# Performance work log

Measured on AMD Instinct MI355X. Metric: run time of the kernel, lower is better.

The kernel has to match this reference:

```python
import jax, jax.numpy as jnp
import numpy as np

N = 50000   # nodes
E = 800000  # edges (avg degree 16)
F = 16      # input node feature dim
H = 64      # hidden_channels
G = 128     # number of graphs
L = 3       # num_layers
OUT = 8     # output_channels


def _glorot(key, shape):
    fan = shape[-2] + shape[-1]
    return jax.random.normal(key, shape, dtype=jnp.float32) * jnp.sqrt(2.0 / fan)


def setup_inputs() -> dict:
    key = jax.random.key(0)
    ks = jax.random.split(key, 16)
    z = lambda *s: jnp.zeros(s, jnp.float32)
    return {
        "x": jax.random.normal(ks[0], (N, F), jnp.float32),
        "pos": jax.random.normal(ks[1], (N, 3), jnp.float32),
        "edge_index": jax.random.randint(ks[2], (2, E), 0, N),
        "batch": jnp.sort(jax.random.randint(ks[3], (N,), 0, G)),
        "node_W1": _glorot(ks[4], (F, H)), "node_b1": z(H),
        "node_W2": _glorot(ks[5], (H, H)), "node_b2": z(H),
        "local_W1": _glorot(ks[6], (L, 2 * H + 3, H)), "local_b1": z(L, H),
        "local_W2": _glorot(ks[7], (L, H, H)), "local_b2": z(L, H),
        "global_W1": _glorot(ks[8], (L, H, H)), "global_b1": z(L, H),
        "global_W2": _glorot(ks[9], (L, H, H)), "global_b2": z(L, H),
        "lin1_W": _glorot(ks[10], (H, H // 2)), "lin1_b": z(H // 2),
        "lin2_W": _glorot(ks[11], (H // 2, OUT)), "lin2_b": z(OUT),
    }


def reference(x, pos, edge_index, batch,
              node_W1, node_b1, node_W2, node_b2,
              local_W1, local_b1, local_W2, local_b2,
              global_W1, global_b1, global_W2, global_b2,
              lin1_W, lin1_b, lin2_W, lin2_b):
    n = x.shape[0]
    src, dst = edge_index[0], edge_index[1]  # x_j = x[src], x_i = x[dst]
    # node_lin: Linear -> ReLU -> Linear
    h = jnp.maximum(x @ node_W1 + node_b1, 0.0) @ node_W2 + node_b2
    for l in range(L):
        # message: cat([x_i, x_j, pos_j]) -> local_nn (Linear, ReLU, Linear)
        m = jnp.concatenate([h[dst], h[src], pos[src]], axis=-1)  # [E, 2H+3]
        m = jnp.maximum(m @ local_W1[l] + local_b1[l], 0.0) @ local_W2[l] + local_b2[l]
        # aggregate: scatter-add over destination nodes
        agg = jax.ops.segment_sum(m, dst, num_segments=n)
        # global_nn (Linear, ReLU, Linear), then outer ReLU from forward loop
        h = jnp.maximum(agg @ global_W1[l] + global_b1[l], 0.0) @ global_W2[l] + global_b2[l]
        h = jnp.maximum(h, 0.0)
    h = jnp.maximum(h @ lin1_W + lin1_b, 0.0)
    out = h @ lin2_W + lin2_b  # [N, OUT]
    # graph readout: scatter-add over batch ids
    return jax.ops.segment_sum(out, batch, num_segments=G)  # [G, OUT]
```

## Files before the change

kernel.cpp:

```cpp
#include <hip/hip_runtime.h>

#define N_NODES 50000
#define N_EDGES 800000
#define NGRAPH  128
#define XPITCH  72
#define NB      391
#define HEPB    4096
#define SEPB    8192
#define NGRP    3125

typedef short bf16x8 __attribute__((ext_vector_type(8)));
typedef float f32x4  __attribute__((ext_vector_type(4)));


__device__ __forceinline__ float atomAddF(float* p, float v) {
#if defined(__gfx950__) || defined(__AMDGCN__)
    return unsafeAtomicAdd(p, v);
#else
    return atomicAdd(p, v);
#endif
}

__device__ __forceinline__ unsigned short f2bf(float x) {
    unsigned u = __builtin_bit_cast(unsigned, x);
    u += 0x7fffu + ((u >> 16) & 1u);
    return (unsigned short)(u >> 16);
}
__device__ __forceinline__ float bf2f(unsigned short h) {
    return __builtin_bit_cast(float, (unsigned)h << 16);
}

__device__ __forceinline__ f32x4 mk4(float b) { f32x4 a = {b, b, b, b}; return a; }

template<int NKC, int KROW>
__device__ __forceinline__ f32x4 w_tile(const bf16x8* a,
                                        const unsigned short* __restrict__ Wm,
                                        int nt, int col, int quad, f32x4 acc) {
    const unsigned short* wp = Wm + (nt * 16 + col) * KROW + quad * 8;
#pragma unroll
    for (int c = 0; c < NKC; ++c) {
        bf16x8 b = *(const bf16x8*)(wp + c * 32);
        acc = __builtin_amdgcn_mfma_f32_16x16x32_bf16(a[c], b, acc, 0, 0, 0);
    }
    return acc;
}

template<int NKC>
__device__ __forceinline__ void a_load(const unsigned short* __restrict__ sl,
                                       int col, int quad, bf16x8* a) {
    a[0] = *(const bf16x8*)(sl + col * XPITCH + quad * 8);
    if (NKC > 1) a[1] = *(const bf16x8*)(sl + col * XPITCH + quad * 8 + 32);
}

__device__ __forceinline__ void w_store1(unsigned short* __restrict__ sl,
                                         int wv, int col, int quad, f32x4 acc,
                                         bool relu) {
#pragma unroll
    for (int r = 0; r < 4; ++r) {
        float x = acc[r];
        if (relu) x = fmaxf(x, 0.f);
        sl[(quad * 4 + r) * XPITCH + wv * 16 + col] = f2bf(x);
    }
}

__device__ __forceinline__ void g_store1(unsigned short* __restrict__ g, int gn0,
                                         int wv, int col, int quad, f32x4 acc) {
#pragma unroll
    for (int r = 0; r < 4; ++r) {
        int node = gn0 + quad * 4 + r;
        if (node < N_NODES)
            g[(size_t)node * 64 + wv * 16 + col] = f2bf(acc[r]);
    }
}

#define OFF_NW1T  0
#define OFF_NW2T  2048
#define OFF_LYR   6144
#define LYR_SZ    20480
#define OFF_LIN1T 67584
#define OFF_LIN2T 69632
#define WT_TOTAL  70144

__global__ __launch_bounds__(256) void kPrep(
    const float* __restrict__ nW1, const float* __restrict__ nW2,
    const float* __restrict__ lW1, const float* __restrict__ lW2,
    const float* __restrict__ gW1, const float* __restrict__ gW2,
    const float* __restrict__ lin1W, const float* __restrict__ lin2W,
    unsigned short* __restrict__ WT, int* __restrict__ gHist,
    float* __restrict__ out) {
    int i = blockIdx.x * 256 + threadIdx.x;
    if (blockIdx.x == 0) {
        for (int k = threadIdx.x; k < NB; k += 256) gHist[k] = 0;
        for (int k = threadIdx.x; k < NGRAPH * 8; k += 256) out[k] = 0.f;
    }
    if (i >= WT_TOTAL) return;
    int j = i;
    if (j < 2048) {
        int n = j >> 5, k = j & 31;
        WT[i] = (k < 16) ? f2bf(nW1[k * 64 + n]) : 0;
        return;
    }
    j -= 2048;
    if (j < 4096) {
        int n = j >> 6, k = j & 63;
        WT[i] = f2bf(nW2[k * 64 + n]);
        return;
    }
    j -= 4096;
    if (j < 3 * LYR_SZ) {
        int l = j / LYR_SZ;  j -= l * LYR_SZ;
        int m = j >> 12;     j &= 4095;
        int n = j >> 6, k = j & 63;
        const float* src;
        if (m == 0)      src = lW1 + (size_t)l * 131 * 64;
        else if (m == 1) src = lW1 + (size_t)l * 131 * 64 + 64 * 64;
        else if (m == 2) src = lW2 + (size_t)l * 4096;
        else if (m == 3) src = gW1 + (size_t)l * 4096;
        else             src = gW2 + (size_t)l * 4096;
        WT[i] = f2bf(src[k * 64 + n]);
        return;
    }
    j -= 3 * LYR_SZ;
    if (j < 2048) {
        int n = j >> 6, k = j & 63;
        WT[i] = f2bf(lin1W[k * 32 + n]);
        return;
    }
    j -= 2048;
    {
        int n = j >> 5, k = j & 31;
        WT[i] = (n < 8) ? f2bf(lin2W[k * 8 + n]) : 0;
    }
}

__global__ __launch_bounds__(256) void kHist(const int* __restrict__ ei,
                                             int* __restrict__ gHist) {
    __shared__ int h[NB];
    int tid = threadIdx.x;
    for (int i = tid; i < NB; i += 256) h[i] = 0;
    __syncthreads();
    int base = blockIdx.x * HEPB;
#pragma unroll
    for (int k = 0; k < HEPB; k += 256) {
        int e = base + k + tid;
        if (e < N_EDGES) atomicAdd(&h[ei[N_EDGES + e] >> 7], 1);
    }
    __syncthreads();
    for (int i = tid; i < NB; i += 256)
        if (h[i]) atomicAdd(&gHist[i], h[i]);
}

__global__ __launch_bounds__(256) void kScanB(const int* __restrict__ gHist,
                                              int* __restrict__ bucketOff,
                                              int* __restrict__ cursor) {
    __shared__ int s0[512], s1[512];
    int tid = threadIdx.x;
    for (int e = tid; e < 512; e += 256) s0[e] = (e < NB) ? gHist[e] : 0;
    __syncthreads();
    int* sp = s0; int* dp = s1;
    for (int off = 1; off < 512; off <<= 1) {
        for (int e = tid; e < 512; e += 256)
            dp[e] = sp[e] + ((e >= off) ? sp[e - off] : 0);
        __syncthreads();
        int* t = sp; sp = dp; dp = t;
    }
    for (int e = tid; e < NB; e += 256) {
        int excl = sp[e] - gHist[e];
        bucketOff[e] = excl;
        cursor[e] = excl;
    }
    if (tid == 0) bucketOff[NB] = sp[NB - 1];
}

__global__ __launch_bounds__(256) void kScat(const int* __restrict__ ei,
                                             int* __restrict__ cursor,
                                             int* __restrict__ packs) {
    __shared__ int sdata[SEPB];
    __shared__ int hist[NB];
    __shared__ int loff[NB + 1];
    __shared__ int gbase[NB];
    __shared__ int sc0[512], sc1[512];
    int tid = threadIdx.x;
    int base = blockIdx.x * SEPB;
    int nE = min(SEPB, N_EDGES - base);

    for (int i = tid; i < NB; i += 256) hist[i] = 0;
    __syncthreads();

    int myPack[SEPB / 256];
    unsigned short myRank[SEPB / 256];
#pragma unroll
    for (int kk = 0; kk < SEPB / 256; ++kk) {
        int e = base + kk * 256 + tid;
        if (e < N_EDGES) {
            int s = ei[e], d = ei[N_EDGES + e];
            myPack[kk] = (s << 16) | d;
            myRank[kk] = (unsigned short)atomicAdd(&hist[d >> 7], 1);
        }
    }
    __syncthreads();

    for (int e = tid; e < 512; e += 256) sc0[e] = (e < NB) ? hist[e] : 0;
    __syncthreads();
    int* sp = sc0; int* dp = sc1;
    for (int off = 1; off < 512; off <<= 1) {
        for (int e = tid; e < 512; e += 256)
            dp[e] = sp[e] + ((e >= off) ? sp[e - off] : 0);
        __syncthreads();
        int* t = sp; sp = dp; dp = t;
    }
    for (int e = tid; e < NB; e += 256) loff[e] = sp[e] - hist[e];
    if (tid == 0) loff[NB] = sp[NB - 1];
    __syncthreads();

    for (int e = tid; e < NB; e += 256)
        gbase[e] = hist[e] ? atomicAdd(&cursor[e], hist[e]) : 0;
#pragma unroll
    for (int kk = 0; kk < SEPB / 256; ++kk) {
        int e = base + kk * 256 + tid;
        if (e < N_EDGES) {
            int p = myPack[kk];
            int b = (p & 0xffff) >> 7;
            sdata[loff[b] + myRank[kk]] = p;
        }
    }
    __syncthreads();

    for (int i = tid; i < nE; i += 256) {
        int p = sdata[i];
        int b = (p & 0xffff) >> 7;
        packs[gbase[b] + (i - loff[b])] = p;
    }
}

__global__ __launch_bounds__(256) void kSortA(
    const int* __restrict__ bucketOff, const int* __restrict__ packs,
    unsigned short* __restrict__ srcList, int* __restrict__ rowPtr,
    const float* __restrict__ x, const float* __restrict__ pos,
    const unsigned short* __restrict__ WT,
    const float* __restrict__ nb1, const float* __restrict__ nb2,
    const float* __restrict__ lW1f, const float* __restrict__ lb1,
    unsigned short* __restrict__ u, unsigned short* __restrict__ v) {
    __shared__ int hist[128];
    __shared__ int cur[128];
    __shared__ int sc0[128], sc1[128];
    __shared__ unsigned short SL[16 * XPITCH];
    __shared__ float pw[48];

    int tid = threadIdx.x;
    if (blockIdx.x < NB) {
        int nbk = blockIdx.x;
        int nodeBase = nbk * 128;
        int nvalid = min(128, N_NODES - nodeBase);
        int eb = bucketOff[nbk], ee = bucketOff[nbk + 1];

        if (tid < 128) hist[tid] = 0;
        __syncthreads();
        for (int i = eb + tid; i < ee; i += 256)
            atomicAdd(&hist[packs[i] & 127], 1);
        __syncthreads();

        if (tid < 128) sc0[tid] = hist[tid];
        __syncthreads();
        int* sp = sc0; int* dp = sc1;
        for (int off = 1; off < 128; off <<= 1) {
            if (tid < 128) dp[tid] = sp[tid] + ((tid >= off) ? sp[tid - off] : 0);
            __syncthreads();
            int* t = sp; sp = dp; dp = t;
        }
        if (tid < 128) {
            int excl = eb + sp[tid] - hist[tid];
            if (tid < nvalid) rowPtr[nodeBase + tid] = excl;
            cur[tid] = excl;
        }
        if (nbk == NB - 1 && tid == 0) rowPtr[N_NODES] = ee;
        __syncthreads();

        for (int i = eb + tid; i < ee; i += 256) {
            int p = packs[i];
            int ps = atomicAdd(&cur[p & 127], 1);
            srcList[ps] = (unsigned short)(((unsigned)p) >> 16);
        }
        return;
    }

    int gn0 = (blockIdx.x - NB) * 16;
    int lane = tid & 63;
    int wv = __builtin_amdgcn_readfirstlane(tid >> 6);
    int col = lane & 15, quad = lane >> 4;

    for (int idx = tid; idx < 512; idx += 256) {
        int m = idx >> 5, k = idx & 31;
        int node = gn0 + m;
        float val = (k < 16 && node < N_NODES) ? x[(size_t)node * 16 + k] : 0.f;
        SL[m * XPITCH + k] = f2bf(val);
    }
    if (tid < 48) {
        int node = gn0 + tid / 3;
        pw[tid] = (node < N_NODES) ? pos[(size_t)node * 3 + tid % 3] : 0.f;
    }
    __syncthreads();

    bf16x8 a[2];
    f32x4 acc;

    a_load<1>(SL, col, quad, a);
    acc = w_tile<1, 32>(a, WT + OFF_NW1T, wv, col, quad, mk4(nb1[wv * 16 + col]));
    __syncthreads();
    w_store1(SL, wv, col, quad, acc, true);
    __syncthreads();

    a_load<2>(SL, col, quad, a);
    acc = w_tile<2, 64>(a, WT + OFF_NW2T, wv, col, quad, mk4(nb2[wv * 16 + col]));
    __syncthreads();
    w_store1(SL, wv, col, quad, acc, false);
    __syncthreads();

    const unsigned short* aT = WT + OFF_LYR;
    const unsigned short* bT = aT + 4096;
    const float* W1c = lW1f + 128 * 64;

    a_load<2>(SL, col, quad, a);
    acc = w_tile<2, 64>(a, aT, wv, col, quad, mk4(0.f));
    g_store1(u, gn0, wv, col, quad, acc);

    int ch = wv * 16 + col;
    acc = w_tile<2, 64>(a, bT, wv, col, quad, mk4(lb1[ch]));
    float w0 = W1c[ch], w1 = W1c[64 + ch], w2 = W1c[128 + ch];
#pragma unroll
    for (int r = 0; r < 4; ++r) {
        int rr = quad * 4 + r;
        acc[r] += pw[rr * 3 + 0] * w0 + pw[rr * 3 + 1] * w1 + pw[rr * 3 + 2] * w2;
    }
    g_store1(v, gn0, wv, col, quad, acc);
}

__global__ __launch_bounds__(256) void kAgg(const int* __restrict__ rowPtr,
                                            const unsigned short* __restrict__ srcList,
                                            const unsigned short* __restrict__ u,
                                            const unsigned short* __restrict__ v,
                                            unsigned short* __restrict__ aggH) {
    int gt = blockIdx.x * 256 + threadIdx.x;
    int n = gt >> 6;
    int lane = gt & 63;
    if (n >= N_NODES) return;
    int sub = lane & 15;
    int q = lane >> 4;

    ushort4 uu = *(const ushort4*)(u + (size_t)n * 64 + sub * 4);
    float u0 = bf2f(uu.x), u1 = bf2f(uu.y), u2 = bf2f(uu.z), u3 = bf2f(uu.w);

    int b = rowPtr[n], e = rowPtr[n + 1];
    int deg = e - b;
    int full16 = deg & ~15;
    float a0 = 0.f, a1 = 0.f, a2 = 0.f, a3 = 0.f;

    for (int g0 = 0; g0 < full16; g0 += 16) {
        int i = b + g0 + 4 * q;
        int s0 = srcList[i];
        int s1 = srcList[i + 1];
        int s2 = srcList[i + 2];
        int s3 = srcList[i + 3];
        ushort4 w0 = *(const ushort4*)(v + (size_t)s0 * 64 + sub * 4);
        ushort4 w1 = *(const ushort4*)(v + (size_t)s1 * 64 + sub * 4);
        ushort4 w2 = *(const ushort4*)(v + (size_t)s2 * 64 + sub * 4);
        ushort4 w3 = *(const ushort4*)(v + (size_t)s3 * 64 + sub * 4);
        a0 += fmaxf(u0 + bf2f(w0.x), 0.f) + fmaxf(u0 + bf2f(w1.x), 0.f)
            + fmaxf(u0 + bf2f(w2.x), 0.f) + fmaxf(u0 + bf2f(w3.x), 0.f);
        a1 += fmaxf(u1 + bf2f(w0.y), 0.f) + fmaxf(u1 + bf2f(w1.y), 0.f)
            + fmaxf(u1 + bf2f(w2.y), 0.f) + fmaxf(u1 + bf2f(w3.y), 0.f);
        a2 += fmaxf(u2 + bf2f(w0.z), 0.f) + fmaxf(u2 + bf2f(w1.z), 0.f)
            + fmaxf(u2 + bf2f(w2.z), 0.f) + fmaxf(u2 + bf2f(w3.z), 0.f);
        a3 += fmaxf(u3 + bf2f(w0.w), 0.f) + fmaxf(u3 + bf2f(w1.w), 0.f)
            + fmaxf(u3 + bf2f(w2.w), 0.f) + fmaxf(u3 + bf2f(w3.w), 0.f);
    }
    for (int i = b + full16 + q; i < e; i += 4) {
        int s0 = srcList[i];
        ushort4 w0 = *(const ushort4*)(v + (size_t)s0 * 64 + sub * 4);
        a0 += fmaxf(u0 + bf2f(w0.x), 0.f);
        a1 += fmaxf(u1 + bf2f(w0.y), 0.f);
        a2 += fmaxf(u2 + bf2f(w0.z), 0.f);
        a3 += fmaxf(u3 + bf2f(w0.w), 0.f);
    }

    a0 += __shfl_xor(a0, 16); a0 += __shfl_xor(a0, 32);
    a1 += __shfl_xor(a1, 16); a1 += __shfl_xor(a1, 32);
    a2 += __shfl_xor(a2, 16); a2 += __shfl_xor(a2, 32);
    a3 += __shfl_xor(a3, 16); a3 += __shfl_xor(a3, 32);

    if (q == 0) {
        ushort4 o;
        o.x = f2bf(a0); o.y = f2bf(a1); o.z = f2bf(a2); o.w = f2bf(a3);
        *(ushort4*)(aggH + (size_t)n * 64 + sub * 4) = o;
    }
}

__global__ __launch_bounds__(256) void kB(
    const float* __restrict__ pos, const int* __restrict__ rowPtr,
    const unsigned short* __restrict__ WT, int l,
    const float* __restrict__ lb2, const float* __restrict__ gb1,
    const float* __restrict__ gb2,
    const float* __restrict__ lW1f_next, const float* __restrict__ b1n,
    unsigned short* __restrict__ u, unsigned short* __restrict__ v) {
    __shared__ unsigned short SL[16 * XPITCH];
    __shared__ float pw[48];
    __shared__ int rp[17];
    int tid = threadIdx.x;
    int lane = tid & 63;
    int wv = __builtin_amdgcn_readfirstlane(tid >> 6);
    int gn0 = blockIdx.x * 16;
    int col = lane & 15, quad = lane >> 4;

    const unsigned short* LYR = WT + OFF_LYR + (size_t)l * LYR_SZ;
    const unsigned short* lW2T = LYR + 2 * 4096;
    const unsigned short* gW1T = LYR + 3 * 4096;
    const unsigned short* gW2T = LYR + 4 * 4096;
    const unsigned short* aTn = WT + OFF_LYR + (size_t)(l + 1) * LYR_SZ;
    const unsigned short* bTn = aTn + 4096;

    const uint4* ag = (const uint4*)(u + (size_t)gn0 * 64);
    if (tid < 128) {
        int m = tid >> 3, sg = tid & 7;
        uint4 d = (gn0 + m < N_NODES) ? ag[tid] : make_uint4(0u, 0u, 0u, 0u);
        *(uint4*)&SL[m * XPITCH + sg * 8] = d;
    }
    if (tid < 48) {
        int node = gn0 + tid / 3;
        pw[tid] = (node < N_NODES) ? pos[(size_t)node * 3 + tid % 3] : 0.f;
    }
    if (tid < 17) rp[tid] = rowPtr[min(gn0 + tid, N_NODES)];
    __syncthreads();

    bf16x8 a[2];
    f32x4 acc;
    float dgr[4];
#pragma unroll
    for (int r = 0; r < 4; ++r)
        dgr[r] = (float)(rp[quad * 4 + r + 1] - rp[quad * 4 + r]);

    {
        float b = lb2[wv * 16 + col];
        f32x4 init = {dgr[0] * b, dgr[1] * b, dgr[2] * b, dgr[3] * b};
        a_load<2>(SL, col, quad, a);
        acc = w_tile<2, 64>(a, lW2T, wv, col, quad, init);
    }
    __syncthreads();
    w_store1(SL, wv, col, quad, acc, false);
    __syncthreads();

    a_load<2>(SL, col, quad, a);
    acc = w_tile<2, 64>(a, gW1T, wv, col, quad, mk4(gb1[wv * 16 + col]));
    __syncthreads();
    w_store1(SL, wv, col, quad, acc, true);
    __syncthreads();

    a_load<2>(SL, col, quad, a);
    acc = w_tile<2, 64>(a, gW2T, wv, col, quad, mk4(gb2[wv * 16 + col]));
    __syncthreads();
    w_store1(SL, wv, col, quad, acc, true);
    __syncthreads();

    a_load<2>(SL, col, quad, a);
    acc = w_tile<2, 64>(a, aTn, wv, col, quad, mk4(0.f));
    g_store1(u, gn0, wv, col, quad, acc);

    const float* W1c = lW1f_next + 128 * 64;
    int ch = wv * 16 + col;
    acc = w_tile<2, 64>(a, bTn, wv, col, quad, mk4(b1n[ch]));
    float w0 = W1c[ch], w1 = W1c[64 + ch], w2 = W1c[128 + ch];
#pragma unroll
    for (int r = 0; r < 4; ++r) {
        int rr = quad * 4 + r;
        acc[r] += pw[rr * 3 + 0] * w0 + pw[rr * 3 + 1] * w1 + pw[rr * 3 + 2] * w2;
    }
    g_store1(v, gn0, wv, col, quad, acc);
}

__global__ __launch_bounds__(256) void kC(
    const int* __restrict__ rowPtr, const int* __restrict__ batch,
    const unsigned short* __restrict__ WT,
    const float* __restrict__ lb2, const float* __restrict__ gb1,
    const float* __restrict__ gb2,
    const float* __restrict__ lin1b, const float* __restrict__ lin2b,
    const unsigned short* __restrict__ u, float* __restrict__ out) {
    __shared__ unsigned short SL[16 * XPITCH];
    __shared__ int rp[17];
    __shared__ int batchW[16];
    __shared__ float bins[16 * 8];
    int tid = threadIdx.x;
    int lane = tid & 63;
    int wv = __builtin_amdgcn_readfirstlane(tid >> 6);
    int gn0 = blockIdx.x * 16;
    int col = lane & 15, quad = lane >> 4;

    const unsigned short* LYR = WT + OFF_LYR + 2 * LYR_SZ;
    const unsigned short* lW2T = LYR + 2 * 4096;
    const unsigned short* gW1T = LYR + 3 * 4096;
    const unsigned short* gW2T = LYR + 4 * 4096;
    const unsigned short* lin1T = WT + OFF_LIN1T;
    const unsigned short* lin2T = WT + OFF_LIN2T;

    const uint4* ag = (const uint4*)(u + (size_t)gn0 * 64);
    if (tid < 128) {
        int m = tid >> 3, sg = tid & 7;
        *(uint4*)&SL[m * XPITCH + sg * 8] = ag[tid];
    }
    if (tid < 17) rp[tid] = rowPtr[gn0 + tid];
    if (tid < 16) batchW[tid] = batch[gn0 + tid];
    if (tid >= 128 && tid < 256) bins[tid - 128] = 0.f;
    __syncthreads();

    bf16x8 a[2];
    f32x4 acc;
    float dgr[4];
#pragma unroll
    for (int r = 0; r < 4; ++r)
        dgr[r] = (float)(rp[quad * 4 + r + 1] - rp[quad * 4 + r]);

    {
        float b = lb2[wv * 16 + col];
        f32x4 init = {dgr[0] * b, dgr[1] * b, dgr[2] * b, dgr[3] * b};
        a_load<2>(SL, col, quad, a);
        acc = w_tile<2, 64>(a, lW2T, wv, col, quad, init);
    }
    __syncthreads();
    w_store1(SL, wv, col, quad, acc, false);
    __syncthreads();

    a_load<2>(SL, col, quad, a);
    acc = w_tile<2, 64>(a, gW1T, wv, col, quad, mk4(gb1[wv * 16 + col]));
    __syncthreads();
    w_store1(SL, wv, col, quad, acc, true);
    __syncthreads();

    a_load<2>(SL, col, quad, a);
    acc = w_tile<2, 64>(a, gW2T, wv, col, quad, mk4(gb2[wv * 16 + col]));
    __syncthreads();
    w_store1(SL, wv, col, quad, acc, true);
    __syncthreads();

    a_load<2>(SL, col, quad, a);
    if (wv < 2)
        acc = w_tile<2, 64>(a, lin1T, wv, col, quad, mk4(lin1b[wv * 16 + col]));
    __syncthreads();
    if (wv < 2) w_store1(SL, wv, col, quad, acc, true);
    __syncthreads();

    if (wv == 0) {
        a_load<1>(SL, col, quad, a);
        f32x4 o = w_tile<1, 32>(a, lin2T, 0, col, quad,
                                mk4(col < 8 ? lin2b[col] : 0.f));
        int gmin = batchW[0];
        if (col < 8) {
#pragma unroll
            for (int r = 0; r < 4; ++r) {
                int nl = quad * 4 + r;
                atomicAdd(&bins[(batchW[nl] - gmin) * 8 + col], o[r]);
            }
        }
    }
    __syncthreads();
    int gmin = batchW[0];
    int nb8 = (batchW[15] - gmin + 1) * 8;
    for (int idx = tid; idx < nb8; idx += 256)
        atomAddF(&out[gmin * 8 + idx], bins[idx]);
}

extern "C" void kernel_launch(void* const* d_in, const int* in_sizes, int n_in,
                              void* d_out, int out_size, void* d_ws, size_t ws_size,
                              hipStream_t stream) {
    const float* x     = (const float*)d_in[0];
    const float* pos   = (const float*)d_in[1];
    const int*   ei    = (const int*)d_in[2];
    const int*   batch = (const int*)d_in[3];
    const float* nW1   = (const float*)d_in[4];
    const float* nb1   = (const float*)d_in[5];
    const float* nW2   = (const float*)d_in[6];
    const float* nb2   = (const float*)d_in[7];
    const float* lW1   = (const float*)d_in[8];
    const float* lb1   = (const float*)d_in[9];
    const float* lW2   = (const float*)d_in[10];
    const float* lb2   = (const float*)d_in[11];
    const float* gW1   = (const float*)d_in[12];
    const float* gb1   = (const float*)d_in[13];
    const float* gW2   = (const float*)d_in[14];
    const float* gb2   = (const float*)d_in[15];
    const float* lin1W = (const float*)d_in[16];
    const float* lin1b = (const float*)d_in[17];
    const float* lin2W = (const float*)d_in[18];
    const float* lin2b = (const float*)d_in[19];
    float* out = (float*)d_out;

    unsigned short* u  = (unsigned short*)d_ws;
    unsigned short* v  = u + (size_t)N_NODES * 64;
    unsigned short* WT = v + (size_t)N_NODES * 64;
    int* gHist = (int*)(WT + WT_TOTAL);
    int* bucketOff = gHist + NB;
    int* cursor = bucketOff + NB + 1;
    int* rowPtr = cursor + NB;
    int* packs = rowPtr + N_NODES + 1;
    unsigned short* srcList = (unsigned short*)(packs + N_EDGES);
    unsigned short* aggH = u;

    const int aggBlocks = (N_NODES * 64 + 255) / 256;

    kPrep<<<(WT_TOTAL + 255) / 256, 256, 0, stream>>>(nW1, nW2, lW1, lW2, gW1, gW2,
                                                      lin1W, lin2W, WT, gHist, out);
    kHist<<<(N_EDGES + HEPB - 1) / HEPB, 256, 0, stream>>>(ei, gHist);
    kScanB<<<1, 256, 0, stream>>>(gHist, bucketOff, cursor);
    kScat<<<(N_EDGES + SEPB - 1) / SEPB, 256, 0, stream>>>(ei, cursor, packs);
    kSortA<<<NB + NGRP, 256, 0, stream>>>(bucketOff, packs, srcList, rowPtr,
                                          x, pos, WT, nb1, nb2, lW1, lb1, u, v);

    for (int l = 0; l < 3; ++l) {
        kAgg<<<aggBlocks, 256, 0, stream>>>(rowPtr, srcList, u, v, aggH);
        if (l < 2) {
            kB<<<NGRP, 256, 0, stream>>>(
                pos, rowPtr, WT, l,
                lb2 + l * 64, gb1 + l * 64, gb2 + l * 64,
                lW1 + (size_t)(l + 1) * 131 * 64, lb1 + (l + 1) * 64,
                u, v);
        } else {
            kC<<<NGRP, 256, 0, stream>>>(
                rowPtr, batch, WT,
                lb2 + l * 64, gb1 + l * 64, gb2 + l * 64,
                lin1b, lin2b, u, out);
        }
    }
}
```

Measured before the change: 292.4 us.

## Replace two-pass bucket sort with per-node counts and atomic scatter CSR build

Builds the CSR by counting in-degree per destination node with global atomics inside the histogram kernel, then scatters each edge's source directly to its row using atomic per-node cursors. The scan is folded into the last block of kHist via a done counter, and the packed intermediate buffer is dropped. This removes the kScanB and kScat launches and the extra pass over packs. The price is many contended global atomics on rowCnt and gCursor, and neighbor order within a row is no longer deterministic, so floating-point sums may vary slightly between runs.

```diff
diff --git a/kernel.cpp b/kernel.cpp
--- a/kernel.cpp
+++ b/kernel.cpp
@@ -6,7 +6,6 @@
 #define XPITCH  72
 #define NB      391
 #define HEPB    4096
-#define SEPB    8192
 #define NGRP    3125
 
 typedef short bf16x8 __attribute__((ext_vector_type(8)));
@@ -87,11 +86,14 @@
     const float* __restrict__ gW1, const float* __restrict__ gW2,
     const float* __restrict__ lin1W, const float* __restrict__ lin2W,
     unsigned short* __restrict__ WT, int* __restrict__ gHist,
+    int* __restrict__ rowCnt, int* __restrict__ doneCnt,
     float* __restrict__ out) {
     int i = blockIdx.x * 256 + threadIdx.x;
+    if (i < N_NODES) rowCnt[i] = 0;
     if (blockIdx.x == 0) {
         for (int k = threadIdx.x; k < NB; k += 256) gHist[k] = 0;
         for (int k = threadIdx.x; k < NGRAPH * 8; k += 256) out[k] = 0.f;
+        if (threadIdx.x == 0) *doneCnt = 0;
     }
     if (i >= WT_TOTAL) return;
     int j = i;
@@ -134,8 +136,13 @@
 }
 
 __global__ __launch_bounds__(256) void kHist(const int* __restrict__ ei,
-                                             int* __restrict__ gHist) {
+                                             int* __restrict__ rowCnt,
+                                             int* __restrict__ gHist,
+                                             int* __restrict__ bucketOff,
+                                             int* __restrict__ doneCnt) {
     __shared__ int h[NB];
+    __shared__ int s0[512], s1[512];
+    __shared__ int amLast;
     int tid = threadIdx.x;
     for (int i = tid; i < NB; i += 256) h[i] = 0;
     __syncthreads();
@@ -143,19 +150,28 @@
 #pragma unroll
     for (int k = 0; k < HEPB; k += 256) {
         int e = base + k + tid;
-        if (e < N_EDGES) atomicAdd(&h[ei[N_EDGES + e] >> 7], 1);
+        if (e < N_EDGES) {
+            int d = ei[N_EDGES + e];
+            atomicAdd(&h[d >> 7], 1);
+            atomicAdd(&rowCnt[d], 1);
+        }
     }
     __syncthreads();
     for (int i = tid; i < NB; i += 256)
         if (h[i]) atomicAdd(&gHist[i], h[i]);
-}
-
-__global__ __launch_bounds__(256) void kScanB(const int* __restrict__ gHist,
-                                              int* __restrict__ bucketOff,
-                                              int* __restrict__ cursor) {
-    __shared__ int s0[512], s1[512];
-    int tid = threadIdx.x;
-    for (int e = tid; e < 512; e += 256) s0[e] = (e < NB) ? gHist[e] : 0;
+
+    __threadfence();
+    if (tid == 0) amLast = (atomicAdd(doneCnt, 1) == (int)gridDim.x - 1);
+    __syncthreads();
+    if (!amLast) return;
+    __threadfence();
+
+    int g0 = 0, g1 = 0;
+    for (int e = tid; e < 512; e += 256) {
+        int vbk = (e < NB) ? atomicAdd(&gHist[e], 0) : 0;
+        if (e < 256) g0 = vbk; else g1 = vbk;
+        s0[e] = vbk;
+    }
     __syncthreads();
     int* sp = s0; int* dp = s1;
     for (int off = 1; off < 512; off <<= 1) {
@@ -164,103 +180,30 @@
         __syncthreads();
         int* t = sp; sp = dp; dp = t;
     }
-    for (int e = tid; e < NB; e += 256) {
-        int excl = sp[e] - gHist[e];
-        bucketOff[e] = excl;
-        cursor[e] = excl;
-    }
+    for (int e = tid; e < NB; e += 256)
+        bucketOff[e] = sp[e] - ((e < 256) ? g0 : g1);
     if (tid == 0) bucketOff[NB] = sp[NB - 1];
 }
 
-__global__ __launch_bounds__(256) void kScat(const int* __restrict__ ei,
-                                             int* __restrict__ cursor,
-                                             int* __restrict__ packs) {
-    __shared__ int sdata[SEPB];
-    __shared__ int hist[NB];
-    __shared__ int loff[NB + 1];
-    __shared__ int gbase[NB];
-    __shared__ int sc0[512], sc1[512];
-    int tid = threadIdx.x;
-    int base = blockIdx.x * SEPB;
-    int nE = min(SEPB, N_EDGES - base);
-
-    for (int i = tid; i < NB; i += 256) hist[i] = 0;
-    __syncthreads();
-
-    int myPack[SEPB / 256];
-    unsigned short myRank[SEPB / 256];
-#pragma unroll
-    for (int kk = 0; kk < SEPB / 256; ++kk) {
-        int e = base + kk * 256 + tid;
-        if (e < N_EDGES) {
-            int s = ei[e], d = ei[N_EDGES + e];
-            myPack[kk] = (s << 16) | d;
-            myRank[kk] = (unsigned short)atomicAdd(&hist[d >> 7], 1);
-        }
-    }
-    __syncthreads();
-
-    for (int e = tid; e < 512; e += 256) sc0[e] = (e < NB) ? hist[e] : 0;
-    __syncthreads();
-    int* sp = sc0; int* dp = sc1;
-    for (int off = 1; off < 512; off <<= 1) {
-        for (int e = tid; e < 512; e += 256)
-            dp[e] = sp[e] + ((e >= off) ? sp[e - off] : 0);
-        __syncthreads();
-        int* t = sp; sp = dp; dp = t;
-    }
-    for (int e = tid; e < NB; e += 256) loff[e] = sp[e] - hist[e];
-    if (tid == 0) loff[NB] = sp[NB - 1];
-    __syncthreads();
-
-    for (int e = tid; e < NB; e += 256)
-        gbase[e] = hist[e] ? atomicAdd(&cursor[e], hist[e]) : 0;
-#pragma unroll
-    for (int kk = 0; kk < SEPB / 256; ++kk) {
-        int e = base + kk * 256 + tid;
-        if (e < N_EDGES) {
-            int p = myPack[kk];
-            int b = (p & 0xffff) >> 7;
-            sdata[loff[b] + myRank[kk]] = p;
-        }
-    }
-    __syncthreads();
-
-    for (int i = tid; i < nE; i += 256) {
-        int p = sdata[i];
-        int b = (p & 0xffff) >> 7;
-        packs[gbase[b] + (i - loff[b])] = p;
-    }
-}
-
-__global__ __launch_bounds__(256) void kSortA(
-    const int* __restrict__ bucketOff, const int* __restrict__ packs,
-    unsigned short* __restrict__ srcList, int* __restrict__ rowPtr,
+__global__ __launch_bounds__(256) void kRowA(
+    const int* __restrict__ rowCnt, const int* __restrict__ bucketOff,
+    int* __restrict__ gCursor, int* __restrict__ rowPtr,
     const float* __restrict__ x, const float* __restrict__ pos,
     const unsigned short* __restrict__ WT,
     const float* __restrict__ nb1, const float* __restrict__ nb2,
     const float* __restrict__ lW1f, const float* __restrict__ lb1,
     unsigned short* __restrict__ u, unsigned short* __restrict__ v) {
-    __shared__ int hist[128];
-    __shared__ int cur[128];
     __shared__ int sc0[128], sc1[128];
     __shared__ unsigned short SL[16 * XPITCH];
     __shared__ float pw[48];
 
     int tid = threadIdx.x;
     if (blockIdx.x < NB) {
-        int nbk = blockIdx.x;
-        int nodeBase = nbk * 128;
+        int b = blockIdx.x;
+        int nodeBase = b * 128;
         int nvalid = min(128, N_NODES - nodeBase);
-        int eb = bucketOff[nbk], ee = bucketOff[nbk + 1];
-
-        if (tid < 128) hist[tid] = 0;
-        __syncthreads();
-        for (int i = eb + tid; i < ee; i += 256)
-            atomicAdd(&hist[packs[i] & 127], 1);
-        __syncthreads();
-
-        if (tid < 128) sc0[tid] = hist[tid];
+        int c = (tid < nvalid) ? rowCnt[nodeBase + tid] : 0;
+        if (tid < 128) sc0[tid] = c;
         __syncthreads();
         int* sp = sc0; int* dp = sc1;
         for (int off = 1; off < 128; off <<= 1) {
@@ -268,19 +211,12 @@
             __syncthreads();
             int* t = sp; sp = dp; dp = t;
         }
-        if (tid < 128) {
-            int excl = eb + sp[tid] - hist[tid];
-            if (tid < nvalid) rowPtr[nodeBase + tid] = excl;
-            cur[tid] = excl;
+        if (tid < nvalid) {
+            int pos = bucketOff[b] + sp[tid] - c;
+            rowPtr[nodeBase + tid] = pos;
+            gCursor[nodeBase + tid] = pos;
         }
-        if (nbk == NB - 1 && tid == 0) rowPtr[N_NODES] = ee;
-        __syncthreads();
-
-        for (int i = eb + tid; i < ee; i += 256) {
-            int p = packs[i];
-            int ps = atomicAdd(&cur[p & 127], 1);
-            srcList[ps] = (unsigned short)(((unsigned)p) >> 16);
-        }
+        if (b == NB - 1 && tid == 0) rowPtr[N_NODES] = bucketOff[NB];
         return;
     }
 
@@ -333,6 +269,21 @@
         acc[r] += pw[rr * 3 + 0] * w0 + pw[rr * 3 + 1] * w1 + pw[rr * 3 + 2] * w2;
     }
     g_store1(v, gn0, wv, col, quad, acc);
+}
+
+__global__ __launch_bounds__(256) void kScatE(const int* __restrict__ ei,
+                                              int* __restrict__ gCursor,
+                                              unsigned short* __restrict__ srcList) {
+    int e = blockIdx.x * 1024 + threadIdx.x;
+#pragma unroll
+    for (int k = 0; k < 4; ++k, e += 256) {
+        if (e < N_EDGES) {
+            int s = ei[e];
+            int d = ei[N_EDGES + e];
+            int pos = atomicAdd(&gCursor[d], 1);
+            srcList[pos] = (unsigned short)s;
+        }
+    }
 }
 
 __global__ __launch_bounds__(256) void kAgg(const int* __restrict__ rowPtr,
@@ -596,21 +547,23 @@
     unsigned short* WT = v + (size_t)N_NODES * 64;
     int* gHist = (int*)(WT + WT_TOTAL);
     int* bucketOff = gHist + NB;
-    int* cursor = bucketOff + NB + 1;
-    int* rowPtr = cursor + NB;
-    int* packs = rowPtr + N_NODES + 1;
-    unsigned short* srcList = (unsigned short*)(packs + N_EDGES);
+    int* rowCnt = bucketOff + NB + 1;
+    int* gCursor = rowCnt + N_NODES;
+    int* rowPtr = gCursor + N_NODES;
+    int* doneCnt = rowPtr + N_NODES + 1;
+    unsigned short* srcList = (unsigned short*)(doneCnt + 1);
     unsigned short* aggH = u;
 
     const int aggBlocks = (N_NODES * 64 + 255) / 256;
 
     kPrep<<<(WT_TOTAL + 255) / 256, 256, 0, stream>>>(nW1, nW2, lW1, lW2, gW1, gW2,
-                                                      lin1W, lin2W, WT, gHist, out);
-    kHist<<<(N_EDGES + HEPB - 1) / HEPB, 256, 0, stream>>>(ei, gHist);
-    kScanB<<<1, 256, 0, stream>>>(gHist, bucketOff, cursor);
-    kScat<<<(N_EDGES + SEPB - 1) / SEPB, 256, 0, stream>>>(ei, cursor, packs);
-    kSortA<<<NB + NGRP, 256, 0, stream>>>(bucketOff, packs, srcList, rowPtr,
-                                          x, pos, WT, nb1, nb2, lW1, lb1, u, v);
+                                                      lin1W, lin2W, WT, gHist,
+                                                      rowCnt, doneCnt, out);
+    kHist<<<(N_EDGES + HEPB - 1) / HEPB, 256, 0, stream>>>(ei, rowCnt, gHist,
+                                                           bucketOff, doneCnt);
+    kRowA<<<NB + NGRP, 256, 0, stream>>>(rowCnt, bucketOff, gCursor, rowPtr,
+                                         x, pos, WT, nb1, nb2, lW1, lb1, u, v);
+    kScatE<<<(N_EDGES + 1023) / 1024, 256, 0, stream>>>(ei, gCursor, srcList);
 
     for (int l = 0; l < 3; ++l) {
         kAgg<<<aggBlocks, 256, 0, stream>>>(rowPtr, srcList, u, v, aggH);
```

Result: slower. 352.6 us (+20.6%).

## Fuse neighbor aggregation into layer kernels and merge the bucket scan into the histogram

Applied to the files above, without the earlier changes.

The separate aggregation kernel is removed. Each block of kB/kC now gathers and sums neighbor messages for its own 16 nodes straight into shared memory before the MLP. The v buffer is double-buffered across layers so a layer never overwrites messages that other blocks still read. The single-block bucket scan is folded into the histogram kernel: the last block to finish, found with an atomic done counter, runs the scan. This removes three launches per forward and the round trip of the aggregated features through global memory. The cost is fewer waves in flight for the latency-bound gather, since each wave now processes 4 nodes one after another.

```diff
diff --git a/kernel.cpp b/kernel.cpp
--- a/kernel.cpp
+++ b/kernel.cpp
@@ -73,6 +73,64 @@
     }
 }
 
+__device__ __forceinline__ void wave_agg4(const int* rp, unsigned short* __restrict__ sl,
+                                          const unsigned short* __restrict__ u,
+                                          const unsigned short* __restrict__ vin,
+                                          const unsigned short* __restrict__ srcList,
+                                          int gn0, int wv, int lane) {
+    int sub = lane & 15, q = lane >> 4;
+#pragma unroll
+    for (int mi = 0; mi < 4; ++mi) {
+        int m = wv * 4 + mi;
+        int n = gn0 + m;
+        ushort4 uu = *(const ushort4*)(u + (size_t)n * 64 + sub * 4);
+        float u0 = bf2f(uu.x), u1 = bf2f(uu.y), u2 = bf2f(uu.z), u3 = bf2f(uu.w);
+        int b = rp[m], e = rp[m + 1];
+        int deg = e - b;
+        int full16 = deg & ~15;
+        float a0 = 0.f, a1 = 0.f, a2 = 0.f, a3 = 0.f;
+
+        for (int g0 = 0; g0 < full16; g0 += 16) {
+            int i = b + g0 + 4 * q;
+            int s0 = srcList[i];
+            int s1 = srcList[i + 1];
+            int s2 = srcList[i + 2];
+            int s3 = srcList[i + 3];
+            ushort4 w0 = *(const ushort4*)(vin + (size_t)s0 * 64 + sub * 4);
+            ushort4 w1 = *(const ushort4*)(vin + (size_t)s1 * 64 + sub * 4);
+            ushort4 w2 = *(const ushort4*)(vin + (size_t)s2 * 64 + sub * 4);
+            ushort4 w3 = *(const ushort4*)(vin + (size_t)s3 * 64 + sub * 4);
+            a0 += fmaxf(u0 + bf2f(w0.x), 0.f) + fmaxf(u0 + bf2f(w1.x), 0.f)
+                + fmaxf(u0 + bf2f(w2.x), 0.f) + fmaxf(u0 + bf2f(w3.x), 0.f);
+            a1 += fmaxf(u1 + bf2f(w0.y), 0.f) + fmaxf(u1 + bf2f(w1.y), 0.f)
+                + fmaxf(u1 + bf2f(w2.y), 0.f) + fmaxf(u1 + bf2f(w3.y), 0.f);
+            a2 += fmaxf(u2 + bf2f(w0.z), 0.f) + fmaxf(u2 + bf2f(w1.z), 0.f)
+                + fmaxf(u2 + bf2f(w2.z), 0.f) + fmaxf(u2 + bf2f(w3.z), 0.f);
+            a3 += fmaxf(u3 + bf2f(w0.w), 0.f) + fmaxf(u3 + bf2f(w1.w), 0.f)
+                + fmaxf(u3 + bf2f(w2.w), 0.f) + fmaxf(u3 + bf2f(w3.w), 0.f);
+        }
+        for (int i = b + full16 + q; i < e; i += 4) {
+            int s0 = srcList[i];
+            ushort4 w0 = *(const ushort4*)(vin + (size_t)s0 * 64 + sub * 4);
+            a0 += fmaxf(u0 + bf2f(w0.x), 0.f);
+            a1 += fmaxf(u1 + bf2f(w0.y), 0.f);
+            a2 += fmaxf(u2 + bf2f(w0.z), 0.f);
+            a3 += fmaxf(u3 + bf2f(w0.w), 0.f);
+        }
+
+        a0 += __shfl_xor(a0, 16); a0 += __shfl_xor(a0, 32);
+        a1 += __shfl_xor(a1, 16); a1 += __shfl_xor(a1, 32);
+        a2 += __shfl_xor(a2, 16); a2 += __shfl_xor(a2, 32);
+        a3 += __shfl_xor(a3, 16); a3 += __shfl_xor(a3, 32);
+
+        if (q == 0) {
+            ushort4 o;
+            o.x = f2bf(a0); o.y = f2bf(a1); o.z = f2bf(a2); o.w = f2bf(a3);
+            *(ushort4*)&sl[m * XPITCH + sub * 4] = o;
+        }
+    }
+}
+
 #define OFF_NW1T  0
 #define OFF_NW2T  2048
 #define OFF_LYR   6144
@@ -87,11 +145,12 @@
     const float* __restrict__ gW1, const float* __restrict__ gW2,
     const float* __restrict__ lin1W, const float* __restrict__ lin2W,
     unsigned short* __restrict__ WT, int* __restrict__ gHist,
-    float* __restrict__ out) {
+    int* __restrict__ doneCnt, float* __restrict__ out) {
     int i = blockIdx.x * 256 + threadIdx.x;
     if (blockIdx.x == 0) {
         for (int k = threadIdx.x; k < NB; k += 256) gHist[k] = 0;
         for (int k = threadIdx.x; k < NGRAPH * 8; k += 256) out[k] = 0.f;
+        if (threadIdx.x == 0) *doneCnt = 0;
     }
     if (i >= WT_TOTAL) return;
     int j = i;
@@ -134,8 +193,13 @@
 }
 
 __global__ __launch_bounds__(256) void kHist(const int* __restrict__ ei,
-                                             int* __restrict__ gHist) {
+                                             int* __restrict__ gHist,
+                                             int* __restrict__ bucketOff,
+                                             int* __restrict__ cursor,
+                                             int* __restrict__ doneCnt) {
     __shared__ int h[NB];
+    __shared__ int s0[512], s1[512];
+    __shared__ int amLast;
     int tid = threadIdx.x;
     for (int i = tid; i < NB; i += 256) h[i] = 0;
     __syncthreads();
@@ -148,14 +212,15 @@
     __syncthreads();
     for (int i = tid; i < NB; i += 256)
         if (h[i]) atomicAdd(&gHist[i], h[i]);
-}
-
-__global__ __launch_bounds__(256) void kScanB(const int* __restrict__ gHist,
-                                              int* __restrict__ bucketOff,
-                                              int* __restrict__ cursor) {
-    __shared__ int s0[512], s1[512];
-    int tid = threadIdx.x;
-    for (int e = tid; e < 512; e += 256) s0[e] = (e < NB) ? gHist[e] : 0;
+
+    __threadfence();
+    if (tid == 0) amLast = (atomicAdd(doneCnt, 1) == (int)gridDim.x - 1);
+    __syncthreads();
+    if (!amLast) return;
+    __threadfence();
+
+    for (int e = tid; e < 512; e += 256)
+        s0[e] = (e < NB) ? atomicAdd(&gHist[e], 0) : 0;
     __syncthreads();
     int* sp = s0; int* dp = s1;
     for (int off = 1; off < 512; off <<= 1) {
@@ -165,7 +230,8 @@
         int* t = sp; sp = dp; dp = t;
     }
     for (int e = tid; e < NB; e += 256) {
-        int excl = sp[e] - gHist[e];
+        int cnt = (e < NB) ? atomicAdd(&gHist[e], 0) : 0;
+        int excl = sp[e] - cnt;
         bucketOff[e] = excl;
         cursor[e] = excl;
     }
@@ -335,73 +401,16 @@
     g_store1(v, gn0, wv, col, quad, acc);
 }
 
-__global__ __launch_bounds__(256) void kAgg(const int* __restrict__ rowPtr,
-                                            const unsigned short* __restrict__ srcList,
-                                            const unsigned short* __restrict__ u,
-                                            const unsigned short* __restrict__ v,
-                                            unsigned short* __restrict__ aggH) {
-    int gt = blockIdx.x * 256 + threadIdx.x;
-    int n = gt >> 6;
-    int lane = gt & 63;
-    if (n >= N_NODES) return;
-    int sub = lane & 15;
-    int q = lane >> 4;
-
-    ushort4 uu = *(const ushort4*)(u + (size_t)n * 64 + sub * 4);
-    float u0 = bf2f(uu.x), u1 = bf2f(uu.y), u2 = bf2f(uu.z), u3 = bf2f(uu.w);
-
-    int b = rowPtr[n], e = rowPtr[n + 1];
-    int deg = e - b;
-    int full16 = deg & ~15;
-    float a0 = 0.f, a1 = 0.f, a2 = 0.f, a3 = 0.f;
-
-    for (int g0 = 0; g0 < full16; g0 += 16) {
-        int i = b + g0 + 4 * q;
-        int s0 = srcList[i];
-        int s1 = srcList[i + 1];
-        int s2 = srcList[i + 2];
-        int s3 = srcList[i + 3];
-        ushort4 w0 = *(const ushort4*)(v + (size_t)s0 * 64 + sub * 4);
-        ushort4 w1 = *(const ushort4*)(v + (size_t)s1 * 64 + sub * 4);
-        ushort4 w2 = *(const ushort4*)(v + (size_t)s2 * 64 + sub * 4);
-        ushort4 w3 = *(const ushort4*)(v + (size_t)s3 * 64 + sub * 4);
-        a0 += fmaxf(u0 + bf2f(w0.x), 0.f) + fmaxf(u0 + bf2f(w1.x), 0.f)
-            + fmaxf(u0 + bf2f(w2.x), 0.f) + fmaxf(u0 + bf2f(w3.x), 0.f);
-        a1 += fmaxf(u1 + bf2f(w0.y), 0.f) + fmaxf(u1 + bf2f(w1.y), 0.f)
-            + fmaxf(u1 + bf2f(w2.y), 0.f) + fmaxf(u1 + bf2f(w3.y), 0.f);
-        a2 += fmaxf(u2 + bf2f(w0.z), 0.f) + fmaxf(u2 + bf2f(w1.z), 0.f)
-            + fmaxf(u2 + bf2f(w2.z), 0.f) + fmaxf(u2 + bf2f(w3.z), 0.f);
-        a3 += fmaxf(u3 + bf2f(w0.w), 0.f) + fmaxf(u3 + bf2f(w1.w), 0.f)
-            + fmaxf(u3 + bf2f(w2.w), 0.f) + fmaxf(u3 + bf2f(w3.w), 0.f);
-    }
-    for (int i = b + full16 + q; i < e; i += 4) {
-        int s0 = srcList[i];
-        ushort4 w0 = *(const ushort4*)(v + (size_t)s0 * 64 + sub * 4);
-        a0 += fmaxf(u0 + bf2f(w0.x), 0.f);
-        a1 += fmaxf(u1 + bf2f(w0.y), 0.f);
-        a2 += fmaxf(u2 + bf2f(w0.z), 0.f);
-        a3 += fmaxf(u3 + bf2f(w0.w), 0.f);
-    }
-
-    a0 += __shfl_xor(a0, 16); a0 += __shfl_xor(a0, 32);
-    a1 += __shfl_xor(a1, 16); a1 += __shfl_xor(a1, 32);
-    a2 += __shfl_xor(a2, 16); a2 += __shfl_xor(a2, 32);
-    a3 += __shfl_xor(a3, 16); a3 += __shfl_xor(a3, 32);
-
-    if (q == 0) {
-        ushort4 o;
-        o.x = f2bf(a0); o.y = f2bf(a1); o.z = f2bf(a2); o.w = f2bf(a3);
-        *(ushort4*)(aggH + (size_t)n * 64 + sub * 4) = o;
-    }
-}
-
 __global__ __launch_bounds__(256) void kB(
     const float* __restrict__ pos, const int* __restrict__ rowPtr,
+    const unsigned short* __restrict__ srcList,
     const unsigned short* __restrict__ WT, int l,
     const float* __restrict__ lb2, const float* __restrict__ gb1,
     const float* __restrict__ gb2,
     const float* __restrict__ lW1f_next, const float* __restrict__ b1n,
-    unsigned short* __restrict__ u, unsigned short* __restrict__ v) {
+    unsigned short* __restrict__ u,
+    const unsigned short* __restrict__ vin,
+    unsigned short* __restrict__ vout) {
     __shared__ unsigned short SL[16 * XPITCH];
     __shared__ float pw[48];
     __shared__ int rp[17];
@@ -418,17 +427,14 @@
     const unsigned short* aTn = WT + OFF_LYR + (size_t)(l + 1) * LYR_SZ;
     const unsigned short* bTn = aTn + 4096;
 
-    const uint4* ag = (const uint4*)(u + (size_t)gn0 * 64);
-    if (tid < 128) {
-        int m = tid >> 3, sg = tid & 7;
-        uint4 d = (gn0 + m < N_NODES) ? ag[tid] : make_uint4(0u, 0u, 0u, 0u);
-        *(uint4*)&SL[m * XPITCH + sg * 8] = d;
-    }
     if (tid < 48) {
         int node = gn0 + tid / 3;
-        pw[tid] = (node < N_NODES) ? pos[(size_t)node * 3 + tid % 3] : 0.f;
-    }
-    if (tid < 17) rp[tid] = rowPtr[min(gn0 + tid, N_NODES)];
+        pw[tid] = pos[(size_t)node * 3 + tid % 3];
+    }
+    if (tid < 17) rp[tid] = rowPtr[gn0 + tid];
+    __syncthreads();
+
+    wave_agg4(rp, SL, u, vin, srcList, gn0, wv, lane);
     __syncthreads();
 
     bf16x8 a[2];
@@ -473,16 +479,17 @@
         int rr = quad * 4 + r;
         acc[r] += pw[rr * 3 + 0] * w0 + pw[rr * 3 + 1] * w1 + pw[rr * 3 + 2] * w2;
     }
-    g_store1(v, gn0, wv, col, quad, acc);
+    g_store1(vout, gn0, wv, col, quad, acc);
 }
 
 __global__ __launch_bounds__(256) void kC(
-    const int* __restrict__ rowPtr, const int* __restrict__ batch,
-    const unsigned short* __restrict__ WT,
+    const int* __restrict__ rowPtr, const unsigned short* __restrict__ srcList,
+    const int* __restrict__ batch, const unsigned short* __restrict__ WT,
     const float* __restrict__ lb2, const float* __restrict__ gb1,
     const float* __restrict__ gb2,
     const float* __restrict__ lin1b, const float* __restrict__ lin2b,
-    const unsigned short* __restrict__ u, float* __restrict__ out) {
+    unsigned short* __restrict__ u, const unsigned short* __restrict__ vin,
+    float* __restrict__ out) {
     __shared__ unsigned short SL[16 * XPITCH];
     __shared__ int rp[17];
     __shared__ int batchW[16];
@@ -500,14 +507,12 @@
     const unsigned short* lin1T = WT + OFF_LIN1T;
     const unsigned short* lin2T = WT + OFF_LIN2T;
 
-    const uint4* ag = (const uint4*)(u + (size_t)gn0 * 64);
-    if (tid < 128) {
-        int m = tid >> 3, sg = tid & 7;
-        *(uint4*)&SL[m * XPITCH + sg * 8] = ag[tid];
-    }
     if (tid < 17) rp[tid] = rowPtr[gn0 + tid];
     if (tid < 16) batchW[tid] = batch[gn0 + tid];
     if (tid >= 128 && tid < 256) bins[tid - 128] = 0.f;
+    __syncthreads();
+
+    wave_agg4(rp, SL, u, vin, srcList, gn0, wv, lane);
     __syncthreads();
 
     bf16x8 a[2];
@@ -592,39 +597,38 @@
     float* out = (float*)d_out;
 
     unsigned short* u  = (unsigned short*)d_ws;
-    unsigned short* v  = u + (size_t)N_NODES * 64;
-    unsigned short* WT = v + (size_t)N_NODES * 64;
+    unsigned short* v0 = u + (size_t)N_NODES * 64;
+    unsigned short* v1 = v0 + (size_t)N_NODES * 64;
+    unsigned short* WT = v1 + (size_t)N_NODES * 64;
     int* gHist = (int*)(WT + WT_TOTAL);
     int* bucketOff = gHist + NB;
     int* cursor = bucketOff + NB + 1;
     int* rowPtr = cursor + NB;
-    int* packs = rowPtr + N_NODES + 1;
+    int* doneCnt = rowPtr + N_NODES + 1;
+    int* packs = doneCnt + 1;
     unsigned short* srcList = (unsigned short*)(packs + N_EDGES);
-    unsigned short* aggH = u;
-
-    const int aggBlocks = (N_NODES * 64 + 255) / 256;
 
     kPrep<<<(WT_TOTAL + 255) / 256, 256, 0, stream>>>(nW1, nW2, lW1, lW2, gW1, gW2,
-                                                      lin1W, lin2W, WT, gHist, out);
-    kHist<<<(N_EDGES + HEPB - 1) / HEPB, 256, 0, stream>>>(ei, gHist);
-    kScanB<<<1, 256, 0, stream>>>(gHist, bucketOff, cursor);
+                                                      lin1W, lin2W, WT, gHist,
+                                                      doneCnt, out);
+    kHist<<<(N_EDGES + HEPB - 1) / HEPB, 256, 0, stream>>>(ei, gHist, bucketOff,
+                                                           cursor, doneCnt);
     kScat<<<(N_EDGES + SEPB - 1) / SEPB, 256, 0, stream>>>(ei, cursor, packs);
     kSortA<<<NB + NGRP, 256, 0, stream>>>(bucketOff, packs, srcList, rowPtr,
-                                          x, pos, WT, nb1, nb2, lW1, lb1, u, v);
-
-    for (int l = 0; l < 3; ++l) {
-        kAgg<<<aggBlocks, 256, 0, stream>>>(rowPtr, srcList, u, v, aggH);
-        if (l < 2) {
-            kB<<<NGRP, 256, 0, stream>>>(
-                pos, rowPtr, WT, l,
-                lb2 + l * 64, gb1 + l * 64, gb2 + l * 64,
-                lW1 + (size_t)(l + 1) * 131 * 64, lb1 + (l + 1) * 64,
-                u, v);
-        } else {
-            kC<<<NGRP, 256, 0, stream>>>(
-                rowPtr, batch, WT,
-                lb2 + l * 64, gb1 + l * 64, gb2 + l * 64,
-                lin1b, lin2b, u, out);
-        }
-    }
-}
+                                          x, pos, WT, nb1, nb2, lW1, lb1, u, v0);
+
+    kB<<<NGRP, 256, 0, stream>>>(
+        pos, rowPtr, srcList, WT, 0,
+        lb2 + 0, gb1 + 0, gb2 + 0,
+        lW1 + (size_t)1 * 131 * 64, lb1 + 64,
+        u, v0, v1);
+    kB<<<NGRP, 256, 0, stream>>>(
+        pos, rowPtr, srcList, WT, 1,
+        lb2 + 64, gb1 + 64, gb2 + 64,
+        lW1 + (size_t)2 * 131 * 64, lb1 + 128,
+        u, v1, v0);
+    kC<<<NGRP, 256, 0, stream>>>(
+        rowPtr, srcList, batch, WT,
+        lb2 + 128, gb1 + 128, gb2 + 128, lin1b, lin2b,
+        u, v0, out);
+}
```

After: 276.3 us. -5.5%, faster.
